# Kernel tuning notes

Measured on AMD Instinct MI355X. Metric: run time of the kernel, lower is better.

## Reference

```python
import jax, jax.numpy as jnp
import numpy as np

N_HEADS = 16

def setup_inputs() -> dict:
    key = jax.random.key(0)
    k1, k2 = jax.random.split(key)
    qkv = jax.random.normal(k1, (4, 3072, 2048), dtype=jnp.float32)
    encoder_kv = jax.random.normal(k2, (4, 2048, 256), dtype=jnp.float32)
    return {"qkv": qkv, "encoder_kv": encoder_kv}

def reference(qkv, encoder_kv):
    bs, width, length = qkv.shape
    ch = width // (3 * N_HEADS)  # 64
    # [bs*H, 3*ch, T] -> q, k, v each [bs*H, ch, T]
    q, k, v = jnp.split(qkv.reshape(bs * N_HEADS, 3 * ch, length), 3, axis=1)
    # encoder kv: [bs, H*2*ch, S] -> ek, ev each [bs*H, ch, S]
    ek, ev = jnp.split(encoder_kv.reshape(bs * N_HEADS, 2 * ch, -1), 2, axis=1)
    k = jnp.concatenate([ek, k], axis=-1)  # [bs*H, ch, S+T]
    v = jnp.concatenate([ev, v], axis=-1)
    scale = ch ** -0.25  # 1/sqrt(sqrt(ch)), applied to both q and k
    weight = jnp.einsum('bct,bcs->bts', q * scale, k * scale)  # [bs*H, T, S+T]
    weight = jax.nn.softmax(weight.astype(jnp.float32), axis=-1).astype(qkv.dtype)
    a = jnp.einsum('bts,bcs->bct', weight, v)  # [bs*H, ch, T]
    return a.reshape(bs, -1, length)
```

## Files before the change

### kernel.cpp

```cpp
#include <hip/hip_runtime.h>
#include <hip/hip_bf16.h>

typedef __attribute__((ext_vector_type(8))) short bf16x8;
typedef __attribute__((ext_vector_type(4))) float f32x4;
typedef __attribute__((ext_vector_type(4))) unsigned u32x4;
typedef __attribute__((ext_vector_type(2))) unsigned u32x2;

#define T_LEN 2048
#define S_ENC 256
#define QSCALE 0.18033688011112042f

#define BARRIER()                                         \
  do {                                                    \
    asm volatile("s_waitcnt lgkmcnt(0)" ::: "memory");    \
    __builtin_amdgcn_s_barrier();                         \
  } while (0)

__device__ __forceinline__ float exp2_hw(float x) {
#if __has_builtin(__builtin_amdgcn_exp2f)
  return __builtin_amdgcn_exp2f(x);
#else
  float r;
  asm("v_exp_f32 %0, %1" : "=v"(r) : "v"(x));
  return r;
#endif
}

__device__ __forceinline__ unsigned cvt_pk_bf16(float lo, float hi) {
  unsigned r;
  asm("v_cvt_pk_bf16_f32 %0, %1, %2" : "=v"(r) : "v"(lo), "v"(hi));
  return r;
}

__device__ __forceinline__ short f2bf(float x) {
  union { __hip_bfloat16 b; short s; } u;
  u.b = __float2bfloat16(x);
  return u.s;
}

__device__ __forceinline__ int swz(int row, int col) {
  return row * 64 + (col ^ ((row & 7) << 3));
}

union PU { u32x4 u; bf16x8 b; };

template<int STRIDE>
__device__ __forceinline__ void tile_body(
    const float* __restrict__ kb, const float* __restrict__ vb, int s0,
    short* __restrict__ Kt, short* __restrict__ Vt,
    const bf16x8 (&qf)[4][2], f32x4 (&o)[4][4], float (&lp)[4], int tid) {

  const int lane = tid & 63;
  const int ln = lane & 15;
  const int lg = lane >> 4;

  const int ks = tid & 63;
  const int kc = (tid >> 6) * 8;
  float kr[8];
  const float* kp = kb + (size_t)kc * STRIDE + (s0 + ks);
#pragma unroll
  for (int r = 0; r < 8; ++r) kr[r] = kp[(size_t)r * STRIDE];

  const int vg = tid & 15;
  const int vc = tid >> 4;
  const float* vp0 = vb + (size_t)vc * STRIDE + (s0 + 4 * vg);
  f32x4 vr0 = *(const f32x4*)(vp0);
  f32x4 vr1 = *(const f32x4*)(vp0 + (size_t)32 * STRIDE);

  BARRIER();

  u32x4 kw;
#pragma unroll
  for (int r = 0; r < 4; ++r) kw[r] = cvt_pk_bf16(kr[2 * r], kr[2 * r + 1]);
  *(u32x4*)(Kt + swz(ks, kc)) = kw;

  const int vcol = 32 * (vg >> 3) + 8 * (vg & 3) + 4 * ((vg >> 2) & 1);
  u32x2 vw0, vw1;
  vw0[0] = cvt_pk_bf16(vr0[0], vr0[1]);
  vw0[1] = cvt_pk_bf16(vr0[2], vr0[3]);
  *(u32x2*)(Vt + swz(vc, vcol)) = vw0;
  vw1[0] = cvt_pk_bf16(vr1[0], vr1[1]);
  vw1[1] = cvt_pk_bf16(vr1[2], vr1[3]);
  *(u32x2*)(Vt + swz(vc + 32, vcol)) = vw1;

  BARRIER();

  bf16x8 kf[4][2];
#pragma unroll
  for (int mt = 0; mt < 4; ++mt) {
    const int row = 16 * mt + ln;
    kf[mt][0] = *(const bf16x8*)(Kt + swz(row, 8 * lg));
    kf[mt][1] = *(const bf16x8*)(Kt + swz(row, 32 + 8 * lg));
  }

  PU pfrag[4][2];
#pragma unroll
  for (int pr = 0; pr < 2; ++pr) {
    f32x4 sacc[2][4];
#pragma unroll
    for (int q2 = 0; q2 < 2; ++q2)
#pragma unroll
      for (int mt = 0; mt < 4; ++mt) sacc[q2][mt] = (f32x4){0.f, 0.f, 0.f, 0.f};

#pragma unroll
    for (int mt = 0; mt < 4; ++mt)
#pragma unroll
      for (int q2 = 0; q2 < 2; ++q2) {
        const int qt = 2 * pr + q2;
        sacc[q2][mt] = __builtin_amdgcn_mfma_f32_16x16x32_bf16(kf[mt][0], qf[qt][0], sacc[q2][mt], 0, 0, 0);
        sacc[q2][mt] = __builtin_amdgcn_mfma_f32_16x16x32_bf16(kf[mt][1], qf[qt][1], sacc[q2][mt], 0, 0, 0);
      }

#pragma unroll
    for (int q2 = 0; q2 < 2; ++q2) {
      const int qt = 2 * pr + q2;
      float pmt[4];
#pragma unroll
      for (int mt = 0; mt < 4; ++mt) {
        float p0 = exp2_hw(sacc[q2][mt][0]);
        float p1 = exp2_hw(sacc[q2][mt][1]);
        float p2 = exp2_hw(sacc[q2][mt][2]);
        float p3 = exp2_hw(sacc[q2][mt][3]);
        pfrag[qt][mt >> 1].u[2 * (mt & 1) + 0] = cvt_pk_bf16(p0, p1);
        pfrag[qt][mt >> 1].u[2 * (mt & 1) + 1] = cvt_pk_bf16(p2, p3);
        pmt[mt] = (p0 + p1) + (p2 + p3);
      }
      lp[qt] += (pmt[0] + pmt[1]) + (pmt[2] + pmt[3]);
    }
  }

#pragma unroll
  for (int sub = 0; sub < 2; ++sub)
#pragma unroll
    for (int ct = 0; ct < 4; ++ct) {
      const bf16x8 vf = *(const bf16x8*)(Vt + swz(16 * ct + ln, 32 * sub + 8 * lg));
#pragma unroll
      for (int qt = 0; qt < 4; ++qt)
        o[qt][ct] = __builtin_amdgcn_mfma_f32_16x16x32_bf16(vf, pfrag[qt][sub].b, o[qt][ct], 0, 0, 0);
    }
}

__global__ __launch_bounds__(512, 2) void attn_kernel(
    const float* __restrict__ qkv, const float* __restrict__ ekv,
    float* __restrict__ out) {
  const int tid = threadIdx.x;
  const int lane = tid & 63;
  const int wave = tid >> 6;
  const int ln = lane & 15;
  const int lg = lane >> 4;

  const int bh = blockIdx.x & 63;
  const int qb = blockIdx.x >> 6;
  const int t0 = qb * 512 + wave * 64;

  const float* qp  = qkv + (size_t)bh * 192 * T_LEN;
  const float* kp  = qp + (size_t)64 * T_LEN;
  const float* vp  = qp + (size_t)128 * T_LEN;
  const float* ekp = ekv + (size_t)bh * 128 * S_ENC;
  const float* evp = ekp + (size_t)64 * S_ENC;

  __shared__ __attribute__((aligned(16))) short Kt[64 * 64];
  __shared__ __attribute__((aligned(16))) short Vt[64 * 64];

  bf16x8 qf[4][2];
#pragma unroll
  for (int qt = 0; qt < 4; ++qt)
#pragma unroll
    for (int kk = 0; kk < 2; ++kk)
#pragma unroll
      for (int j = 0; j < 8; ++j)
        qf[qt][kk][j] =
            f2bf(qp[(size_t)(32 * kk + 8 * lg + j) * T_LEN + (t0 + 16 * qt + ln)] * QSCALE);

  f32x4 o[4][4];
#pragma unroll
  for (int qt = 0; qt < 4; ++qt)
#pragma unroll
    for (int ct = 0; ct < 4; ++ct) o[qt][ct] = (f32x4){0.f, 0.f, 0.f, 0.f};
  float lp[4] = {0.f, 0.f, 0.f, 0.f};

  for (int st = 0; st < 4; ++st)
    tile_body<S_ENC>(ekp, evp, 64 * st, Kt, Vt, qf, o, lp, tid);
  for (int st = 0; st < 32; ++st)
    tile_body<T_LEN>(kp, vp, 64 * st, Kt, Vt, qf, o, lp, tid);

#pragma unroll
  for (int qt = 0; qt < 4; ++qt) {
    float l = lp[qt];
    l += __shfl_xor(l, 16);
    l += __shfl_xor(l, 32);
    const float inv = 1.0f / l;
    float* ob = out + (size_t)bh * 64 * T_LEN + (t0 + 16 * qt + ln);
#pragma unroll
    for (int ct = 0; ct < 4; ++ct)
#pragma unroll
      for (int r = 0; r < 4; ++r)
        ob[(size_t)(16 * ct + 4 * lg + r) * T_LEN] = o[qt][ct][r] * inv;
  }
}

extern "C" void kernel_launch(void* const* d_in, const int* in_sizes, int n_in,
                              void* d_out, int out_size, void* d_ws, size_t ws_size,
                              hipStream_t stream) {
  const float* qkv = (const float*)d_in[0];
  const float* ekv = (const float*)d_in[1];
  float* out = (float*)d_out;
  attn_kernel<<<dim3(256), dim3(512), 0, stream>>>(qkv, ekv, out);
}
```

Before: 88.15 us.

## Use 256-thread blocks with 512 blocks, each thread staging twice the K/V tile

```diff
diff --git a/kernel.cpp b/kernel.cpp
--- a/kernel.cpp
+++ b/kernel.cpp
@@ -56,16 +56,21 @@
 
   const int ks = tid & 63;
   const int kc = (tid >> 6) * 8;
-  float kr[8];
+  float kr[8], kr2[8];
   const float* kp = kb + (size_t)kc * STRIDE + (s0 + ks);
+  const float* kp2 = kp + (size_t)32 * STRIDE;
 #pragma unroll
   for (int r = 0; r < 8; ++r) kr[r] = kp[(size_t)r * STRIDE];
+#pragma unroll
+  for (int r = 0; r < 8; ++r) kr2[r] = kp2[(size_t)r * STRIDE];
 
   const int vg = tid & 15;
   const int vc = tid >> 4;
   const float* vp0 = vb + (size_t)vc * STRIDE + (s0 + 4 * vg);
   f32x4 vr0 = *(const f32x4*)(vp0);
   f32x4 vr1 = *(const f32x4*)(vp0 + (size_t)32 * STRIDE);
+  f32x4 vr2 = *(const f32x4*)(vp0 + (size_t)16 * STRIDE);
+  f32x4 vr3 = *(const f32x4*)(vp0 + (size_t)48 * STRIDE);
 
   BARRIER();
 
@@ -73,15 +78,25 @@
 #pragma unroll
   for (int r = 0; r < 4; ++r) kw[r] = cvt_pk_bf16(kr[2 * r], kr[2 * r + 1]);
   *(u32x4*)(Kt + swz(ks, kc)) = kw;
+  u32x4 kw2;
+#pragma unroll
+  for (int r = 0; r < 4; ++r) kw2[r] = cvt_pk_bf16(kr2[2 * r], kr2[2 * r + 1]);
+  *(u32x4*)(Kt + swz(ks, kc + 32)) = kw2;
 
   const int vcol = 32 * (vg >> 3) + 8 * (vg & 3) + 4 * ((vg >> 2) & 1);
-  u32x2 vw0, vw1;
-  vw0[0] = cvt_pk_bf16(vr0[0], vr0[1]);
-  vw0[1] = cvt_pk_bf16(vr0[2], vr0[3]);
-  *(u32x2*)(Vt + swz(vc, vcol)) = vw0;
-  vw1[0] = cvt_pk_bf16(vr1[0], vr1[1]);
-  vw1[1] = cvt_pk_bf16(vr1[2], vr1[3]);
-  *(u32x2*)(Vt + swz(vc + 32, vcol)) = vw1;
+  u32x2 vw;
+  vw[0] = cvt_pk_bf16(vr0[0], vr0[1]);
+  vw[1] = cvt_pk_bf16(vr0[2], vr0[3]);
+  *(u32x2*)(Vt + swz(vc, vcol)) = vw;
+  vw[0] = cvt_pk_bf16(vr1[0], vr1[1]);
+  vw[1] = cvt_pk_bf16(vr1[2], vr1[3]);
+  *(u32x2*)(Vt + swz(vc + 32, vcol)) = vw;
+  vw[0] = cvt_pk_bf16(vr2[0], vr2[1]);
+  vw[1] = cvt_pk_bf16(vr2[2], vr2[3]);
+  *(u32x2*)(Vt + swz(vc + 16, vcol)) = vw;
+  vw[0] = cvt_pk_bf16(vr3[0], vr3[1]);
+  vw[1] = cvt_pk_bf16(vr3[2], vr3[3]);
+  *(u32x2*)(Vt + swz(vc + 48, vcol)) = vw;
 
   BARRIER();
 
@@ -140,7 +155,7 @@
     }
 }
 
-__global__ __launch_bounds__(512, 2) void attn_kernel(
+__global__ __launch_bounds__(256, 2) void attn_kernel(
     const float* __restrict__ qkv, const float* __restrict__ ekv,
     float* __restrict__ out) {
   const int tid = threadIdx.x;
@@ -151,7 +166,7 @@
 
   const int bh = blockIdx.x & 63;
   const int qb = blockIdx.x >> 6;
-  const int t0 = qb * 512 + wave * 64;
+  const int t0 = qb * 256 + wave * 64;
 
   const float* qp  = qkv + (size_t)bh * 192 * T_LEN;
   const float* kp  = qp + (size_t)64 * T_LEN;
@@ -205,5 +220,5 @@
   const float* qkv = (const float*)d_in[0];
   const float* ekv = (const float*)d_in[1];
   float* out = (float*)d_out;
-  attn_kernel<<<dim3(256), dim3(512), 0, stream>>>(qkv, ekv, out);
-}
+  attn_kernel<<<dim3(512), dim3(256), 0, stream>>>(qkv, ekv, out);
+}
```

Measured after the change: 90.12 us. 2.2% more time.
